# Kernel optimization log

Hardware: AMD Instinct MI355X
Metric: run time of the kernel (lower is better)

## Reference

```python
import jax, jax.numpy as jnp
import numpy as np

# ---- static config (matches init_kwargs) ----
B, NPG, C, L, H = 128, 256, 128, 3, 4   # graphs, nodes/graph, hidden, layers, heads
IN_CH, WALK, EDGE_IN, DEG = 30, 20, 11, 8
N = B * NPG
E = N * DEG
EPG = E // B                             # edges per graph
BN_EPS = 1e-5
HD = C // H


def setup_inputs() -> dict:
    key = jax.random.key(0)
    ks = list(jax.random.split(key, 80))
    ki = iter(ks)
    def w(shape, s=0.05):
        return jax.random.normal(next(ki), shape, jnp.float32) * s
    x = jax.random.normal(next(ki), (N, IN_CH), jnp.float32)
    # edges strictly within each graph (block-diagonal structure)
    src_l = jax.random.randint(next(ki), (E,), 0, NPG)
    dst_l = jax.random.randint(next(ki), (E,), 0, NPG)
    eg = jnp.repeat(jnp.arange(B, dtype=jnp.int32), EPG)
    edge_index = jnp.stack([eg * NPG + src_l.astype(jnp.int32),
                            eg * NPG + dst_l.astype(jnp.int32)])
    edge_attr = jax.random.normal(next(ki), (E, EDGE_IN), jnp.float32)
    batch = jnp.repeat(jnp.arange(B, dtype=jnp.int32), NPG)
    # all Linear weights stored [in, out] so y = x @ W + b
    inp = dict(x=x, edge_attr=edge_attr,
        in_W=w((IN_CH + WALK, C)), in_b=jnp.zeros((C,)),
        ep_W=w((EDGE_IN, C)), ep_b=jnp.zeros((C,)),
        ge_W=w((L, C, C)), ge_b=jnp.zeros((L, C)),          # GINE edge lin
        g1_W=w((L, C, C)), g1_b=jnp.zeros((L, C)),          # GINE nn layer1
        g2_W=w((L, C, C)), g2_b=jnp.zeros((L, C)),          # GINE nn layer2
        qkv_W=w((L, C, 3 * C)), qkv_b=jnp.zeros((L, 3 * C)),
        o_W=w((L, C, C)), o_b=jnp.zeros((L, C)),
        bn1_g=jnp.ones((L, C)), bn1_b=jnp.zeros((L, C)), bn1_m=w((L, C), 0.1), bn1_v=jnp.ones((L, C)),
        bn2_g=jnp.ones((L, C)), bn2_b=jnp.zeros((L, C)), bn2_m=w((L, C), 0.1), bn2_v=jnp.ones((L, C)),
        bn3_g=jnp.ones((L, C)), bn3_b=jnp.zeros((L, C)), bn3_m=w((L, C), 0.1), bn3_v=jnp.ones((L, C)),
        m1_W=w((L, C, 2 * C)), m1_b=jnp.zeros((L, 2 * C)),  # GPS ff block
        m2_W=w((L, 2 * C, C)), m2_b=jnp.zeros((L, C)),
        h1_W=w((C, 64)), h1_b=jnp.zeros((64,)),
        h2_W=w((64, 1)), h2_b=jnp.zeros((1,)),
        edge_index=edge_index, batch=batch)
    return inp


def _bn(x, g, b, m, v):  # BatchNorm1d, inference mode
    return (x - m) * jax.lax.rsqrt(v + BN_EPS) * g + b


def _rwse(edge_index):
    """diag of k-step random-walk matrix per graph; [N, WALK]."""
    src, dst = edge_index
    g = src // NPG
    A = jnp.zeros((B, NPG, NPG), jnp.float32).at[g, src % NPG, dst % NPG].add(1.0)
    A = A + jnp.eye(NPG, dtype=jnp.float32)          # add_self_loops
    deg = jnp.clip(jnp.sum(A, axis=-1), 1.0)         # out-degree of source
    M = jnp.swapaxes(A / deg[..., None], -1, -2)     # M[c,r] = A[r,c]/deg[r]
    p0 = jnp.broadcast_to(jnp.eye(NPG, dtype=jnp.float32), (B, NPG, NPG))
    def step(p, _):
        p = jnp.einsum('bcr,brn->bcn', M, p)
        return p, jnp.diagonal(p, axis1=-2, axis2=-1)
    _, diags = jax.lax.scan(step, p0, None, length=WALK)  # [WALK, B, NPG]
    return jnp.transpose(diags, (1, 2, 0)).reshape(N, WALK)


def _forward(x, edge_attr, in_W, in_b, ep_W, ep_b, ge_W, ge_b, g1_W, g1_b, g2_W, g2_b,
             qkv_W, qkv_b, o_W, o_b,
             bn1_g, bn1_b, bn1_m, bn1_v, bn2_g, bn2_b, bn2_m, bn2_v, bn3_g, bn3_b, bn3_m, bn3_v,
             m1_W, m1_b, m2_W, m2_b, h1_W, h1_b, h2_W, h2_b, edge_index, batch):
    pe = _rwse(edge_index)
    h = jnp.concatenate([x, pe], axis=-1) @ in_W + in_b      # input_proj
    e_emb = edge_attr @ ep_W + ep_b                          # edge_proj (dim==11)
    src, dst = edge_index[0], edge_index[1]
    for i in range(L):
        # --- GINEConv: relu(x_j + lin(edge)) -> scatter-sum -> MLP; eps=0 ---
        e = e_emb @ ge_W[i] + ge_b[i]
        msg = jax.nn.relu(h[src] + e)
        aggr = jax.ops.segment_sum(msg, dst, num_segments=N)
        loc = jax.nn.relu((h + aggr) @ g1_W[i] + g1_b[i]) @ g2_W[i] + g2_b[i]
        h1 = _bn(loc + h, bn1_g[i], bn1_b[i], bn1_m[i], bn1_v[i])
        # --- global multi-head attention on dense batch (uniform n, no padding) ---
        hd = h.reshape(B, NPG, C)
        qkv = hd @ qkv_W[i] + qkv_b[i]
        q, k, v = jnp.split(qkv, 3, axis=-1)
        q = q.reshape(B, NPG, H, HD); k = k.reshape(B, NPG, H, HD); v = v.reshape(B, NPG, H, HD)
        scores = jnp.einsum('bqhd,bkhd->bhqk', q, k) * (HD ** -0.5)
        attn = jax.nn.softmax(scores, axis=-1)
        o = jnp.einsum('bhqk,bkhd->bqhd', attn, v).reshape(B, NPG, C)
        o = (o @ o_W[i] + o_b[i]).reshape(N, C)
        h2 = _bn(o + h, bn2_g[i], bn2_b[i], bn2_m[i], bn2_v[i])
        # --- combine + feed-forward block ---
        out = h1 + h2
        ff = jax.nn.relu(out @ m1_W[i] + m1_b[i]) @ m2_W[i] + m2_b[i]
        h = _bn(out + ff, bn3_g[i], bn3_b[i], bn3_m[i], bn3_v[i])
    # --- global mean pool + head ---
    cnt = jax.ops.segment_sum(jnp.ones((N,), jnp.float32), batch, num_segments=B)
    pooled = jax.ops.segment_sum(h, batch, num_segments=B) / cnt[:, None]
    out = jax.nn.relu(pooled @ h1_W + h1_b) @ h2_W + h2_b
    return out[:, 0]  # [B]


def reference(x, edge_attr, in_W, in_b, ep_W, ep_b, ge_W, ge_b, g1_W, g1_b, g2_W, g2_b,
              qkv_W, qkv_b, o_W, o_b,
              bn1_g, bn1_b, bn1_m, bn1_v, bn2_g, bn2_b, bn2_m, bn2_v, bn3_g, bn3_b, bn3_m, bn3_v,
              m1_W, m1_b, m2_W, m2_b, h1_W, h1_b, h2_W, h2_b, edge_index, batch):
    return _forward(x, edge_attr, in_W, in_b, ep_W, ep_b, ge_W, ge_b, g1_W, g1_b, g2_W, g2_b,
                    qkv_W, qkv_b, o_W, o_b,
                    bn1_g, bn1_b, bn1_m, bn1_v, bn2_g, bn2_b, bn2_m, bn2_v, bn3_g, bn3_b, bn3_m, bn3_v,
                    m1_W, m1_b, m2_W, m2_b, h1_W, h1_b, h2_W, h2_b, edge_index, batch)
```

## Files before the change

### kernel.cpp

```cpp
#include <hip/hip_runtime.h>

#define GN   128
#define GP   256
#define NN   32768
#define NEDGE 262144
#define WALKN 20

typedef __attribute__((ext_vector_type(8))) short bfrag;
typedef __attribute__((ext_vector_type(4))) float ffrag;

__device__ __forceinline__ ushort f2b(float f){
  unsigned u = __float_as_uint(f);
  u += 0x7fffu + ((u >> 16) & 1u);
  return (ushort)(u >> 16);
}

__global__ __launch_bounds__(256) void build_edges(const int* __restrict__ ei, float* __restrict__ A,
                                                   int* __restrict__ epos, int* __restrict__ Ecnt){
  int e = blockIdx.x*256 + threadIdx.x;
  int s = ei[e], d = ei[NEDGE + e];
  int g = s >> 8;
  atomicAdd(&A[((size_t)g<<16) + ((size_t)(s&255)<<8) + (size_t)(d&255)], 1.0f);
  epos[e] = atomicAdd(&Ecnt[d], 1);
}

__global__ __launch_bounds__(256) void pack_edges(const int* __restrict__ ei, const float* __restrict__ ea,
                                                  const int* __restrict__ epos, float* __restrict__ pk){
  int e = blockIdx.x*256 + threadIdx.x;
  int d = ei[NEDGE + e];
  int pos = epos[e];
  if (pos >= 32) return;
  float* dst = pk + ((size_t)d*32 + pos)*12;
  dst[0] = __int_as_float(ei[e]);
  const float* s = ea + (size_t)e*11;
  #pragma unroll
  for (int t = 0; t < 11; t++) dst[1+t] = s[t];
}

__global__ __launch_bounds__(256) void rwse_deg(float* __restrict__ A, float* __restrict__ deg){
  int g = blockIdx.x, r = threadIdx.x;
  float* row = A + ((size_t)g<<16) + ((size_t)r<<8);
  row[r] += 1.0f;
  float s = 0.f;
  for (int c = 0; c < 256; c += 4){
    float4 v = *(const float4*)&row[c];
    s += v.x + v.y + v.z + v.w;
  }
  deg[(g<<8)+r] = fmaxf(s, 1.0f);
}

__global__ __launch_bounds__(256) void prep_m(const float* __restrict__ A, const float* __restrict__ deg,
                                              ushort* __restrict__ Mbf){
  __shared__ float As[64][65];
  __shared__ float Bs[64][65];
  __shared__ float invd[256];
  int g = blockIdx.x;
  const float* Ag = A + ((size_t)g<<16);
  int tid = threadIdx.x, tx = tid & 63, ty = tid >> 6;
  invd[tid] = 1.f / deg[(g<<8)+tid];
  ushort* Mg = Mbf + ((size_t)g<<16);
  const int pr[10] = {0,0,0,0,1,1,1,2,2,3};
  const int pc[10] = {0,1,2,3,1,2,3,2,3,3};
  for (int t = 0; t < 10; t++){
    int R0 = pr[t]*64, C0 = pc[t]*64;
    __syncthreads();
    #pragma unroll
    for (int i = 0; i < 16; i++){
      As[ty + i*4][tx] = Ag[(size_t)(R0 + ty + i*4)*256 + C0 + tx];
      Bs[ty + i*4][tx] = Ag[(size_t)(C0 + ty + i*4)*256 + R0 + tx];
    }
    __syncthreads();
    #pragma unroll
    for (int i = 0; i < 16; i++){
      int cl = ty + i*4;
      Mg[(size_t)(C0+cl)*256 + R0+tx] = f2b(As[tx][cl] * invd[R0+tx]);
      if (R0 != C0)
        Mg[(size_t)(R0+cl)*256 + C0+tx] = f2b(Bs[tx][cl] * invd[C0+tx]);
    }
  }
}

__global__ __launch_bounds__(256, 2) void rwse_mf(const ushort* __restrict__ Mbf,
                                                  float* __restrict__ pe){
  __shared__ __align__(16) ushort Pt[64*264];
  int bid = blockIdx.x;
  int g  = (bid & 7)*16 + (bid >> 5);
  int cb = ((bid >> 3) & 3) << 6;
  int tid = threadIdx.x, lane = tid & 63, w = tid >> 6;
  int l15 = lane & 15, quad = lane >> 4;
  const ushort* Mg = Mbf + ((size_t)g << 16);
  uint4 z4; z4.x = z4.y = z4.z = z4.w = 0u;
  for (int i = tid; i < 2112; i += 256) reinterpret_cast<uint4*>(Pt)[i] = z4;
  __syncthreads();
  if (tid < 64) Pt[tid*264 + cb + tid] = 0x3F80;
  __syncthreads();

  for (int s = 0; s < WALKN; s++){
    ffrag acc[4][4];
    #pragma unroll
    for (int mi = 0; mi < 4; mi++)
      #pragma unroll
      for (int n = 0; n < 4; n++) acc[mi][n] = (ffrag){0.f,0.f,0.f,0.f};
    for (int k0 = 0; k0 < 256; k0 += 32){
      bfrag a[4], b[4];
      #pragma unroll
      for (int mi = 0; mi < 4; mi++)
        a[mi] = *reinterpret_cast<const bfrag*>(&Mg[(size_t)(w*64 + mi*16 + l15)*256 + k0 + quad*8]);
      #pragma unroll
      for (int n = 0; n < 4; n++)
        b[n] = *reinterpret_cast<const bfrag*>(&Pt[(n*16 + l15)*264 + k0 + quad*8]);
      #pragma unroll
      for (int mi = 0; mi < 4; mi++)
        #pragma unroll
        for (int n = 0; n < 4; n++)
          acc[mi][n] = __builtin_amdgcn_mfma_f32_16x16x32_bf16(a[mi], b[n], acc[mi][n], 0, 0, 0);
    }
    __syncthreads();
    #pragma unroll
    for (int mi = 0; mi < 4; mi++){
      int rbase = w*64 + mi*16 + quad*4;
      #pragma unroll
      for (int n = 0; n < 4; n++){
        int cl = n*16 + l15;
        int dd = cb + cl - rbase;
        if (dd >= 0 && dd < 4){
          float dv = (dd==0)?acc[mi][n][0]:(dd==1)?acc[mi][n][1]:(dd==2)?acc[mi][n][2]:acc[mi][n][3];
          pe[(size_t)((g<<8) + cb + cl)*WALKN + s] = dv;
        }
        ushort4 pkk;
        pkk.x = f2b(acc[mi][n][0]); pkk.y = f2b(acc[mi][n][1]);
        pkk.z = f2b(acc[mi][n][2]); pkk.w = f2b(acc[mi][n][3]);
        *reinterpret_cast<ushort4*>(&Pt[cl*264 + rbase]) = pkk;
      }
    }
    __syncthreads();
  }
}

__global__ __launch_bounds__(256) void concat_kernel(const float* __restrict__ x, const float* __restrict__ pe,
                                                     float* __restrict__ xin){
  int idx = blockIdx.x*256 + threadIdx.x;
  int row = idx >> 6, c = idx & 63;
  float v = 0.f;
  if (c < 30) v = x[(size_t)row*30 + c];
  else if (c < 50) v = pe[(size_t)row*20 + (c-30)];
  xin[idx] = v;
}

__global__ __launch_bounds__(256) void prep_wt(const float* __restrict__ in_W, const float* __restrict__ g1_W,
                                               const float* __restrict__ g2_W, const float* __restrict__ qkv_W,
                                               const float* __restrict__ o_W, const float* __restrict__ m1_W,
                                               const float* __restrict__ m2_W, ushort* __restrict__ wt){
  int rgn = blockIdx.y;
  const float* src; int K, N, Kp; size_t dst;
  if (rgn == 0){ src = in_W; K=50; N=128; Kp=64; dst = 0; }
  else if (rgn <= 3){ int i=rgn-1;  src = g1_W + (size_t)i*16384; K=128; N=128; Kp=128; dst = 8192   + (size_t)i*16384; }
  else if (rgn <= 6){ int i=rgn-4;  src = g2_W + (size_t)i*16384; K=128; N=128; Kp=128; dst = 57344  + (size_t)i*16384; }
  else if (rgn <= 9){ int i=rgn-7;  src = qkv_W+ (size_t)i*49152; K=128; N=384; Kp=128; dst = 106496 + (size_t)i*49152; }
  else if (rgn <= 12){ int i=rgn-10; src = o_W  + (size_t)i*16384; K=128; N=128; Kp=128; dst = 253952 + (size_t)i*16384; }
  else if (rgn <= 15){ int i=rgn-13; src = m1_W + (size_t)i*32768; K=128; N=256; Kp=128; dst = 303104 + (size_t)i*32768; }
  else               { int i=rgn-16; src = m2_W + (size_t)i*32768; K=256; N=128; Kp=256; dst = 401408 + (size_t)i*32768; }
  int sz = N * Kp;
  int idx = blockIdx.x*256 + threadIdx.x;
  if (idx >= sz) return;
  int n = idx / Kp, kp = idx - n*Kp;
  float v = (kp < K) ? src[(size_t)kp*N + n] : 0.f;
  wt[dst + idx] = f2b(v);
}

template<int CINP, bool RELU, bool BN, bool HAS_X2, bool HAS_R, bool HAS_R2>
__global__ __launch_bounds__(256, 2) void gemm_mf(
    const float* __restrict__ X1, const float* __restrict__ X2,
    const ushort* __restrict__ WT, const float* __restrict__ bias,
    const float* __restrict__ Rp, const float* __restrict__ R2p,
    const float* __restrict__ bng, const float* __restrict__ bnb,
    const float* __restrict__ bnm, const float* __restrict__ bnv,
    float* __restrict__ Y, int ldY, int colTiles)
{
  constexpr int KT = (CINP > 128) ? 128 : CINP;
  constexpr int XS = KT + 8;
  __shared__ ushort XA[64 * XS];
  __shared__ ushort WS[128 * XS];
  int bt = blockIdx.x;
  int row0 = (bt / colTiles) * 64;
  int c0   = (bt % colTiles) * 128;
  int tid = threadIdx.x;
  int lane = tid & 63, wave = tid >> 6;
  int l15 = lane & 15, quad = lane >> 4;
  int wr = wave >> 1, wc = wave & 1;

  ffrag acc[2][4];
  #pragma unroll
  for (int m = 0; m < 2; m++)
    #pragma unroll
    for (int n = 0; n < 4; n++)
      acc[m][n] = (ffrag){0.f,0.f,0.f,0.f};

  #pragma unroll
  for (int s = 0; s < CINP/KT; s++){
    constexpr int F4PR = KT/4;
    #pragma unroll
    for (int it = 0; it < (64*F4PR)/256; it++){
      int idx = tid + it*256;
      int r = idx / F4PR, c4 = idx % F4PR;
      float4 v = *(const float4*)&X1[(size_t)(row0+r)*CINP + s*KT + c4*4];
      if (HAS_X2){
        float4 w = *(const float4*)&X2[(size_t)(row0+r)*CINP + s*KT + c4*4];
        v.x += w.x; v.y += w.y; v.z += w.z; v.w += w.w;
      }
      ushort4 b; b.x = f2b(v.x); b.y = f2b(v.y); b.z = f2b(v.z); b.w = f2b(v.w);
      *reinterpret_cast<ushort4*>(&XA[r*XS + c4*4]) = b;
    }
    constexpr int U4PR = KT/8;
    #pragma unroll
    for (int it = 0; it < (128*U4PR)/256; it++){
      int idx = tid + it*256;
      int n = idx / U4PR, c8 = idx % U4PR;
      uint4 v = *(const uint4*)&WT[(size_t)(c0+n)*CINP + s*KT + c8*8];
      *reinterpret_cast<uint4*>(&WS[n*XS + c8*8]) = v;
    }
    __syncthreads();
    #pragma unroll
    for (int ks = 0; ks < KT/32; ks++){
      bfrag a[2], b[4];
      #pragma unroll
      for (int m = 0; m < 2; m++)
        a[m] = *reinterpret_cast<const bfrag*>(&XA[(32*wr + 16*m + l15)*XS + ks*32 + quad*8]);
      #pragma unroll
      for (int n = 0; n < 4; n++)
        b[n] = *reinterpret_cast<const bfrag*>(&WS[(64*wc + 16*n + l15)*XS + ks*32 + quad*8]);
      #pragma unroll
      for (int m = 0; m < 2; m++)
        #pragma unroll
        for (int n = 0; n < 4; n++)
          acc[m][n] = __builtin_amdgcn_mfma_f32_16x16x32_bf16(a[m], b[n], acc[m][n], 0, 0, 0);
    }
    __syncthreads();
  }
  #pragma unroll
  for (int m = 0; m < 2; m++)
    #pragma unroll
    for (int n = 0; n < 4; n++){
      int col = c0 + 64*wc + 16*n + l15;
      float bs = bias[col];
      float bnscale = 0.f, bnsh = 0.f;
      if (BN){ bnscale = rsqrtf(bnv[col] + 1e-5f) * bng[col]; bnsh = bnb[col] - bnm[col]*bnscale; }
      #pragma unroll
      for (int rg = 0; rg < 4; rg++){
        int r = row0 + 32*wr + 16*m + quad*4 + rg;
        float v = acc[m][n][rg] + bs;
        if (RELU) v = fmaxf(v, 0.f);
        if (HAS_R) v += Rp[(size_t)r*ldY + col];
        if (BN)   v = v*bnscale + bnsh;
        if (HAS_R2) v += R2p[(size_t)r*ldY + col];
        Y[(size_t)r*ldY + col] = v;
      }
    }
}

__global__ __launch_bounds__(256) void wp_all(const float* __restrict__ epW, const float* __restrict__ epb,
                                              const float* __restrict__ geW, const float* __restrict__ geb,
                                              float* __restrict__ Wp, float* __restrict__ bp){
  int i = blockIdx.x;
  const float* gw = geW + (size_t)i*16384;
  float* wp = Wp + (size_t)i*1408;
  int tid = threadIdx.x;
  for (int idx = tid; idx < 1408; idx += 256){
    int t = idx >> 7, c = idx & 127;
    float s = 0.f;
    for (int k = 0; k < 128; k++) s += epW[t*128+k] * gw[(size_t)k*128 + c];
    wp[idx] = s;
  }
  if (tid < 128){
    float s = geb[(size_t)i*128 + tid];
    for (int k = 0; k < 128; k++) s += epb[k] * gw[(size_t)k*128 + tid];
    bp[(size_t)i*128 + tid] = s;
  }
}

__global__ __launch_bounds__(256) void gine_aggr2(const float* __restrict__ h, const float* __restrict__ pk,
                                                  const int* __restrict__ Ecnt,
                                                  const float* __restrict__ Wp, const float* __restrict__ bp,
                                                  float* __restrict__ aggr){
  int n = blockIdx.x*2 + (threadIdx.x >> 7);
  int ch = threadIdx.x & 127;
  int cnt = Ecnt[n]; if (cnt > 32) cnt = 32;
  float wreg[11];
  #pragma unroll
  for (int t = 0; t < 11; t++) wreg[t] = Wp[t*128 + ch];
  float bpc = bp[ch];
  const float* pkn = pk + (size_t)n*384;
  float acc = 0.f;
  int j = 0;
  for (; j + 4 <= cnt; j += 4){
    const float* p0 = pkn + (size_t)(j+0)*12;
    const float* p1 = pkn + (size_t)(j+1)*12;
    const float* p2 = pkn + (size_t)(j+2)*12;
    const float* p3 = pkn + (size_t)(j+3)*12;
    int s0 = __float_as_int(p0[0]), s1 = __float_as_int(p1[0]);
    int s2 = __float_as_int(p2[0]), s3 = __float_as_int(p3[0]);
    float h0 = h[(size_t)s0*128 + ch];
    float h1 = h[(size_t)s1*128 + ch];
    float h2 = h[(size_t)s2*128 + ch];
    float h3 = h[(size_t)s3*128 + ch];
    float e0 = bpc, e1 = bpc, e2 = bpc, e3 = bpc;
    #pragma unroll
    for (int t = 0; t < 11; t++){
      e0 += p0[1+t]*wreg[t]; e1 += p1[1+t]*wreg[t];
      e2 += p2[1+t]*wreg[t]; e3 += p3[1+t]*wreg[t];
    }
    acc += fmaxf(h0+e0, 0.f) + fmaxf(h1+e1, 0.f) + fmaxf(h2+e2, 0.f) + fmaxf(h3+e3, 0.f);
  }
  for (; j < cnt; j++){
    const float* p0 = pkn + (size_t)j*12;
    int s0 = __float_as_int(p0[0]);
    float h0 = h[(size_t)s0*128 + ch];
    float e0 = bpc;
    #pragma unroll
    for (int t = 0; t < 11; t++) e0 += p0[1+t]*wreg[t];
    acc += fmaxf(h0+e0, 0.f);
  }
  aggr[(size_t)n*128 + ch] = acc;
}

__global__ __launch_bounds__(256, 2) void attn_mf(const float* __restrict__ qkv, float* __restrict__ o){
  __shared__ ushort Ks[256 * 40];
  __shared__ ushort Vt[32 * 264];
  __shared__ ushort PA[4 * 16 * 264];
  int g = blockIdx.x >> 2, hh = blockIdx.x & 3;
  int tid = threadIdx.x, lane = tid & 63, w = tid >> 6;
  int l15 = lane & 15, quad = lane >> 4;
  const float* base = qkv + (size_t)(g<<8)*384;

  #pragma unroll
  for (int it = 0; it < 8; it++){
    int idx = tid + it*256;
    int key = idx >> 3, d4 = idx & 7;
    float4 kv = *(const float4*)&base[(size_t)key*384 + 128 + hh*32 + d4*4];
    ushort4 kb; kb.x=f2b(kv.x); kb.y=f2b(kv.y); kb.z=f2b(kv.z); kb.w=f2b(kv.w);
    *reinterpret_cast<ushort4*>(&Ks[key*40 + d4*4]) = kb;
    float4 vv = *(const float4*)&base[(size_t)key*384 + 256 + hh*32 + d4*4];
    Vt[(d4*4+0)*264 + key] = f2b(vv.x);
    Vt[(d4*4+1)*264 + key] = f2b(vv.y);
    Vt[(d4*4+2)*264 + key] = f2b(vv.z);
    Vt[(d4*4+3)*264 + key] = f2b(vv.w);
  }
  bfrag qf[4];
  #pragma unroll
  for (int qg = 0; qg < 4; qg++){
    int q = w*64 + qg*16 + l15;
    const float* qp = base + (size_t)q*384 + hh*32 + quad*8;
    float4 v0 = *(const float4*)qp;
    float4 v1 = *(const float4*)(qp + 4);
    bfrag t;
    t[0]=(short)f2b(v0.x); t[1]=(short)f2b(v0.y); t[2]=(short)f2b(v0.z); t[3]=(short)f2b(v0.w);
    t[4]=(short)f2b(v1.x); t[5]=(short)f2b(v1.y); t[6]=(short)f2b(v1.z); t[7]=(short)f2b(v1.w);
    qf[qg] = t;
  }
  __syncthreads();

  ushort* pw = &PA[w * 16 * 264];
  const float sc_ = 0.17677669529663687f;
  for (int qg = 0; qg < 4; qg++){
    ffrag sc[16];
    #pragma unroll
    for (int kg = 0; kg < 16; kg++){
      bfrag bk = *reinterpret_cast<const bfrag*>(&Ks[(kg*16 + l15)*40 + quad*8]);
      ffrag z = (ffrag){0.f,0.f,0.f,0.f};
      sc[kg] = __builtin_amdgcn_mfma_f32_16x16x32_bf16(qf[qg], bk, z, 0, 0, 0);
    }
    float inv_l[4];
    #pragma unroll
    for (int rg = 0; rg < 4; rg++){
      float m = sc[0][rg];
      #pragma unroll
      for (int kg = 1; kg < 16; kg++) m = fmaxf(m, sc[kg][rg]);
      #pragma unroll
      for (int off = 1; off < 16; off <<= 1) m = fmaxf(m, __shfl_xor(m, off, 16));
      float ssum = 0.f;
      #pragma unroll
      for (int kg = 0; kg < 16; kg++){
        float p = __expf((sc[kg][rg] - m) * sc_);
        sc[kg][rg] = p; ssum += p;
      }
      #pragma unroll
      for (int off = 1; off < 16; off <<= 1) ssum += __shfl_xor(ssum, off, 16);
      inv_l[rg] = 1.f / ssum;
    }
    #pragma unroll
    for (int kg = 0; kg < 16; kg++)
      #pragma unroll
      for (int rg = 0; rg < 4; rg++)
        pw[(quad*4 + rg)*264 + kg*16 + l15] = f2b(sc[kg][rg]);
    ffrag oa[2];
    oa[0] = (ffrag){0.f,0.f,0.f,0.f};
    oa[1] = (ffrag){0.f,0.f,0.f,0.f};
    #pragma unroll
    for (int ks = 0; ks < 8; ks++){
      bfrag pa = *reinterpret_cast<const bfrag*>(&pw[l15*264 + ks*32 + quad*8]);
      #pragma unroll
      for (int n16 = 0; n16 < 2; n16++){
        bfrag bv = *reinterpret_cast<const bfrag*>(&Vt[(n16*16 + l15)*264 + ks*32 + quad*8]);
        oa[n16] = __builtin_amdgcn_mfma_f32_16x16x32_bf16(pa, bv, oa[n16], 0, 0, 0);
      }
    }
    #pragma unroll
    for (int n16 = 0; n16 < 2; n16++)
      #pragma unroll
      for (int rg = 0; rg < 4; rg++){
        int q = w*64 + qg*16 + quad*4 + rg;
        int col = hh*32 + n16*16 + l15;
        o[((size_t)(g<<8) + q)*128 + col] = oa[n16][rg] * inv_l[rg];
      }
  }
}

__global__ __launch_bounds__(256) void head_kernel(const float* __restrict__ h,
                                                   const float* __restrict__ W1, const float* __restrict__ b1,
                                                   const float* __restrict__ W2, const float* __restrict__ b2,
                                                   float* __restrict__ out){
  int g = blockIdx.x, tid = threadIdx.x;
  int c = tid & 127, half = tid >> 7;
  __shared__ float part[2][128];
  __shared__ float pool[128];
  __shared__ float hid[64];
  float s = 0.f;
  for (int n = half*128; n < half*128 + 128; n++)
    s += h[(size_t)((g<<8)+n)*128 + c];
  part[half][c] = s;
  __syncthreads();
  if (tid < 128) pool[tid] = (part[0][tid] + part[1][tid]) * (1.f/256.f);
  __syncthreads();
  if (tid < 64){
    float v = b1[tid];
    for (int k = 0; k < 128; k++) v += pool[k] * W1[k*64 + tid];
    hid[tid] = fmaxf(v, 0.f);
  }
  __syncthreads();
  if (tid == 0){
    float v = b2[0];
    for (int k = 0; k < 64; k++) v += hid[k] * W2[k];
    out[g] = v;
  }
}

extern "C" void kernel_launch(void* const* d_in, const int* in_sizes, int n_in,
                              void* d_out, int out_size, void* d_ws, size_t ws_size,
                              hipStream_t stream){
  (void)in_sizes; (void)n_in; (void)out_size; (void)ws_size;
  const float* x      = (const float*)d_in[0];
  const float* eattr  = (const float*)d_in[1];
  const float* in_W   = (const float*)d_in[2];
  const float* in_b   = (const float*)d_in[3];
  const float* ep_W   = (const float*)d_in[4];
  const float* ep_b   = (const float*)d_in[5];
  const float* ge_W   = (const float*)d_in[6];
  const float* ge_b   = (const float*)d_in[7];
  const float* g1_W   = (const float*)d_in[8];
  const float* g1_b   = (const float*)d_in[9];
  const float* g2_W   = (const float*)d_in[10];
  const float* g2_b   = (const float*)d_in[11];
  const float* qkv_W  = (const float*)d_in[12];
  const float* qkv_b  = (const float*)d_in[13];
  const float* o_W    = (const float*)d_in[14];
  const float* o_b    = (const float*)d_in[15];
  const float* bn1g = (const float*)d_in[16]; const float* bn1b = (const float*)d_in[17];
  const float* bn1m = (const float*)d_in[18]; const float* bn1v = (const float*)d_in[19];
  const float* bn2g = (const float*)d_in[20]; const float* bn2b = (const float*)d_in[21];
  const float* bn2m = (const float*)d_in[22]; const float* bn2v = (const float*)d_in[23];
  const float* bn3g = (const float*)d_in[24]; const float* bn3b = (const float*)d_in[25];
  const float* bn3m = (const float*)d_in[26]; const float* bn3v = (const float*)d_in[27];
  const float* m1_W = (const float*)d_in[28]; const float* m1_b = (const float*)d_in[29];
  const float* m2_W = (const float*)d_in[30]; const float* m2_b = (const float*)d_in[31];
  const float* h1_W = (const float*)d_in[32]; const float* h1_b = (const float*)d_in[33];
  const float* h2_W = (const float*)d_in[34]; const float* h2_b = (const float*)d_in[35];
  const int*   ei   = (const int*)d_in[36];
  float* out = (float*)d_out;
  float* ws  = (float*)d_ws;
  int*   wsi = (int*)d_ws;

  const size_t oA    = 0;
  const size_t oMbf  = 8388608;
  const size_t oXin  = 0;
  const size_t oQKV  = 0;
  const size_t oT2   = 0;
  const size_t oPk   = 12582912;
  const size_t oDeg  = 25165824;
  const size_t oPe   = 25198592;
  const size_t oH    = 25853952;
  const size_t oB1   = 30048256;
  const size_t oHO   = 34242560;
  const size_t oWp   = 38436864;
  const size_t oBp   = 38441088;
  const size_t oEpos = 38441472;
  const size_t oEcnt = 38703616;
  const size_t oWT   = 38736384;
  ushort* wt  = (ushort*)(ws + oWT);
  ushort* mbf = (ushort*)(ws + oMbf);

  hipMemsetAsync(ws + oA, 0, 8388608*sizeof(float), stream);
  hipMemsetAsync(wsi + oEcnt, 0, 32768*sizeof(int), stream);
  build_edges<<<NEDGE/256, 256, 0, stream>>>(ei, ws+oA, wsi+oEpos, wsi+oEcnt);
  pack_edges<<<NEDGE/256, 256, 0, stream>>>(ei, eattr, wsi+oEpos, ws+oPk);
  rwse_deg<<<GN, 256, 0, stream>>>(ws+oA, ws+oDeg);
  prep_m<<<GN, 256, 0, stream>>>(ws+oA, ws+oDeg, mbf);
  rwse_mf<<<GN*4, 256, 0, stream>>>(mbf, ws+oPe);

  prep_wt<<<dim3(192, 19), 256, 0, stream>>>(in_W, g1_W, g2_W, qkv_W, o_W, m1_W, m2_W, wt);

  concat_kernel<<<NN*64/256, 256, 0, stream>>>(x, ws+oPe, ws+oXin);
  gemm_mf<64,false,false,false,false,false><<<512, 256, 0, stream>>>(
      ws+oXin, nullptr, wt + 0, in_b, nullptr, nullptr, nullptr, nullptr, nullptr, nullptr,
      ws+oH, 128, 1);

  wp_all<<<3, 256, 0, stream>>>(ep_W, ep_b, ge_W, ge_b, ws+oWp, ws+oBp);

  for (int i = 0; i < 3; i++){
    gine_aggr2<<<NN/2, 256, 0, stream>>>(ws+oH, ws+oPk, wsi+oEcnt,
                                         ws+oWp + (size_t)i*1408, ws+oBp + (size_t)i*128, ws+oB1);
    gemm_mf<128,true,false,true,false,false><<<512, 256, 0, stream>>>(
        ws+oH, ws+oB1, wt + 8192 + (size_t)i*16384, g1_b + (size_t)i*128,
        nullptr, nullptr, nullptr, nullptr, nullptr, nullptr, ws+oB1, 128, 1);
    gemm_mf<128,false,true,false,true,false><<<512, 256, 0, stream>>>(
        ws+oB1, nullptr, wt + 57344 + (size_t)i*16384, g2_b + (size_t)i*128,
        ws+oH, nullptr, bn1g+(size_t)i*128, bn1b+(size_t)i*128, bn1m+(size_t)i*128, bn1v+(size_t)i*128,
        ws+oHO, 128, 1);
    gemm_mf<128,false,false,false,false,false><<<1536, 256, 0, stream>>>(
        ws+oH, nullptr, wt + 106496 + (size_t)i*49152, qkv_b + (size_t)i*384,
        nullptr, nullptr, nullptr, nullptr, nullptr, nullptr, ws+oQKV, 384, 3);
    attn_mf<<<GN*4, 256, 0, stream>>>(ws+oQKV, ws+oB1);
    gemm_mf<128,false,true,false,true,true><<<512, 256, 0, stream>>>(
        ws+oB1, nullptr, wt + 253952 + (size_t)i*16384, o_b + (size_t)i*128,
        ws+oH, ws+oHO, bn2g+(size_t)i*128, bn2b+(size_t)i*128, bn2m+(size_t)i*128, bn2v+(size_t)i*128,
        ws+oHO, 128, 1);
    gemm_mf<128,true,false,false,false,false><<<1024, 256, 0, stream>>>(
        ws+oHO, nullptr, wt + 303104 + (size_t)i*32768, m1_b + (size_t)i*256,
        nullptr, nullptr, nullptr, nullptr, nullptr, nullptr, ws+oT2, 256, 2);
    gemm_mf<256,false,true,false,true,false><<<512, 256, 0, stream>>>(
        ws+oT2, nullptr, wt + 401408 + (size_t)i*32768, m2_b + (size_t)i*128,
        ws+oHO, nullptr, bn3g+(size_t)i*128, bn3b+(size_t)i*128, bn3m+(size_t)i*128, bn3v+(size_t)i*128,
        ws+oH, 128, 1);
  }

  head_kernel<<<GN, 256, 0, stream>>>(ws+oH, h1_W, h1_b, h2_W, h2_b, out);
}
```

Measured before the change: 825.3 us.

## Store activations in bf16 and fuse GINE MLP and attention-output/FF GEMM chains

Switches intermediate activations (hidden state, QKV, attention output, aggregation) from fp32 to bf16 storage, halving memory traffic in gathers and GEMM loads. Fuses the two GINE MLP GEMMs into one kernel and the out-projection, FF1 and FF2 GEMMs into another, keeping intermediates in shared memory. This removes several launches and global round-trips at the cost of large LDS use (occupancy 1 for the FF kernel) and extra bf16 rounding error.

Result: faster. 737.7 us (-10.6%).

```diff
diff --git a/kernel.cpp b/kernel.cpp
--- a/kernel.cpp
+++ b/kernel.cpp
@@ -13,6 +13,14 @@
   unsigned u = __float_as_uint(f);
   u += 0x7fffu + ((u >> 16) & 1u);
   return (ushort)(u >> 16);
+}
+__device__ __forceinline__ float b2f(ushort u){
+  return __uint_as_float(((unsigned)u) << 16);
+}
+__device__ __forceinline__ unsigned addpair(unsigned a, unsigned b){
+  float alo = __uint_as_float(a << 16), ahi = __uint_as_float(a & 0xffff0000u);
+  float blo = __uint_as_float(b << 16), bhi = __uint_as_float(b & 0xffff0000u);
+  return ((unsigned)f2b(ahi + bhi) << 16) | (unsigned)f2b(alo + blo);
 }
 
 __global__ __launch_bounds__(256) void build_edges(const int* __restrict__ ei, float* __restrict__ A,
@@ -138,13 +146,13 @@
 }
 
 __global__ __launch_bounds__(256) void concat_kernel(const float* __restrict__ x, const float* __restrict__ pe,
-                                                     float* __restrict__ xin){
+                                                     ushort* __restrict__ xinb){
   int idx = blockIdx.x*256 + threadIdx.x;
   int row = idx >> 6, c = idx & 63;
   float v = 0.f;
   if (c < 30) v = x[(size_t)row*30 + c];
   else if (c < 50) v = pe[(size_t)row*20 + (c-30)];
-  xin[idx] = v;
+  xinb[idx] = f2b(v);
 }
 
 __global__ __launch_bounds__(256) void prep_wt(const float* __restrict__ in_W, const float* __restrict__ g1_W,
@@ -168,17 +176,12 @@
   wt[dst + idx] = f2b(v);
 }
 
-template<int CINP, bool RELU, bool BN, bool HAS_X2, bool HAS_R, bool HAS_R2>
-__global__ __launch_bounds__(256, 2) void gemm_mf(
-    const float* __restrict__ X1, const float* __restrict__ X2,
-    const ushort* __restrict__ WT, const float* __restrict__ bias,
-    const float* __restrict__ Rp, const float* __restrict__ R2p,
-    const float* __restrict__ bng, const float* __restrict__ bnb,
-    const float* __restrict__ bnm, const float* __restrict__ bnv,
-    float* __restrict__ Y, int ldY, int colTiles)
+template<int CINP>
+__global__ __launch_bounds__(256, 2) void gemm_b(
+    const ushort* __restrict__ X1, const ushort* __restrict__ WT,
+    const float* __restrict__ bias, ushort* __restrict__ Y, int ldY, int colTiles)
 {
-  constexpr int KT = (CINP > 128) ? 128 : CINP;
-  constexpr int XS = KT + 8;
+  constexpr int XS = CINP + 8;
   __shared__ ushort XA[64 * XS];
   __shared__ ushort WS[128 * XS];
   int bt = blockIdx.x;
@@ -188,54 +191,42 @@
   int lane = tid & 63, wave = tid >> 6;
   int l15 = lane & 15, quad = lane >> 4;
   int wr = wave >> 1, wc = wave & 1;
-
+  constexpr int C8 = CINP/8;
+
+  #pragma unroll
+  for (int it = 0; it < CINP/32; it++){
+    int idx = tid + it*256;
+    int r = idx / C8, c8 = (idx % C8)*8;
+    *reinterpret_cast<uint4*>(&XA[r*XS + c8]) =
+        *reinterpret_cast<const uint4*>(&X1[(size_t)(row0+r)*CINP + c8]);
+  }
+  #pragma unroll
+  for (int it = 0; it < CINP/16; it++){
+    int idx = tid + it*256;
+    int n = idx / C8, c8 = (idx % C8)*8;
+    *reinterpret_cast<uint4*>(&WS[n*XS + c8]) =
+        *reinterpret_cast<const uint4*>(&WT[(size_t)(c0+n)*CINP + c8]);
+  }
+  __syncthreads();
   ffrag acc[2][4];
   #pragma unroll
   for (int m = 0; m < 2; m++)
     #pragma unroll
+    for (int n = 0; n < 4; n++) acc[m][n] = (ffrag){0.f,0.f,0.f,0.f};
+  #pragma unroll
+  for (int ks = 0; ks < CINP/32; ks++){
+    bfrag a[2], b[4];
+    #pragma unroll
+    for (int m = 0; m < 2; m++)
+      a[m] = *reinterpret_cast<const bfrag*>(&XA[(32*wr + 16*m + l15)*XS + ks*32 + quad*8]);
+    #pragma unroll
     for (int n = 0; n < 4; n++)
-      acc[m][n] = (ffrag){0.f,0.f,0.f,0.f};
-
-  #pragma unroll
-  for (int s = 0; s < CINP/KT; s++){
-    constexpr int F4PR = KT/4;
-    #pragma unroll
-    for (int it = 0; it < (64*F4PR)/256; it++){
-      int idx = tid + it*256;
-      int r = idx / F4PR, c4 = idx % F4PR;
-      float4 v = *(const float4*)&X1[(size_t)(row0+r)*CINP + s*KT + c4*4];
-      if (HAS_X2){
-        float4 w = *(const float4*)&X2[(size_t)(row0+r)*CINP + s*KT + c4*4];
-        v.x += w.x; v.y += w.y; v.z += w.z; v.w += w.w;
-      }
-      ushort4 b; b.x = f2b(v.x); b.y = f2b(v.y); b.z = f2b(v.z); b.w = f2b(v.w);
-      *reinterpret_cast<ushort4*>(&XA[r*XS + c4*4]) = b;
-    }
-    constexpr int U4PR = KT/8;
-    #pragma unroll
-    for (int it = 0; it < (128*U4PR)/256; it++){
-      int idx = tid + it*256;
-      int n = idx / U4PR, c8 = idx % U4PR;
-      uint4 v = *(const uint4*)&WT[(size_t)(c0+n)*CINP + s*KT + c8*8];
-      *reinterpret_cast<uint4*>(&WS[n*XS + c8*8]) = v;
-    }
-    __syncthreads();
-    #pragma unroll
-    for (int ks = 0; ks < KT/32; ks++){
-      bfrag a[2], b[4];
-      #pragma unroll
-      for (int m = 0; m < 2; m++)
-        a[m] = *reinterpret_cast<const bfrag*>(&XA[(32*wr + 16*m + l15)*XS + ks*32 + quad*8]);
+      b[n] = *reinterpret_cast<const bfrag*>(&WS[(64*wc + 16*n + l15)*XS + ks*32 + quad*8]);
+    #pragma unroll
+    for (int m = 0; m < 2; m++)
       #pragma unroll
       for (int n = 0; n < 4; n++)
-        b[n] = *reinterpret_cast<const bfrag*>(&WS[(64*wc + 16*n + l15)*XS + ks*32 + quad*8]);
-      #pragma unroll
-      for (int m = 0; m < 2; m++)
-        #pragma unroll
-        for (int n = 0; n < 4; n++)
-          acc[m][n] = __builtin_amdgcn_mfma_f32_16x16x32_bf16(a[m], b[n], acc[m][n], 0, 0, 0);
-    }
-    __syncthreads();
+        acc[m][n] = __builtin_amdgcn_mfma_f32_16x16x32_bf16(a[m], b[n], acc[m][n], 0, 0, 0);
   }
   #pragma unroll
   for (int m = 0; m < 2; m++)
@@ -243,17 +234,278 @@
     for (int n = 0; n < 4; n++){
       int col = c0 + 64*wc + 16*n + l15;
       float bs = bias[col];
-      float bnscale = 0.f, bnsh = 0.f;
-      if (BN){ bnscale = rsqrtf(bnv[col] + 1e-5f) * bng[col]; bnsh = bnb[col] - bnm[col]*bnscale; }
       #pragma unroll
       for (int rg = 0; rg < 4; rg++){
         int r = row0 + 32*wr + 16*m + quad*4 + rg;
-        float v = acc[m][n][rg] + bs;
-        if (RELU) v = fmaxf(v, 0.f);
-        if (HAS_R) v += Rp[(size_t)r*ldY + col];
-        if (BN)   v = v*bnscale + bnsh;
-        if (HAS_R2) v += R2p[(size_t)r*ldY + col];
-        Y[(size_t)r*ldY + col] = v;
+        Y[(size_t)r*ldY + col] = f2b(acc[m][n][rg] + bs);
+      }
+    }
+}
+
+__global__ __launch_bounds__(256, 2) void gine_mlp(
+    const ushort* __restrict__ hb, const ushort* __restrict__ agb,
+    const ushort* __restrict__ w1, const float* __restrict__ b1v,
+    const ushort* __restrict__ w2, const float* __restrict__ b2v,
+    const float* __restrict__ bng, const float* __restrict__ bnb,
+    const float* __restrict__ bnm, const float* __restrict__ bnv,
+    ushort* __restrict__ h1b)
+{
+  __shared__ ushort XA[64*136];
+  __shared__ ushort WS[128*136];
+  __shared__ ushort T1[64*136];
+  int row0 = blockIdx.x * 64;
+  int tid = threadIdx.x, lane = tid & 63, wave = tid >> 6;
+  int l15 = lane & 15, quad = lane >> 4;
+  int wr = wave >> 1, wc = wave & 1;
+
+  #pragma unroll
+  for (int it = 0; it < 4; it++){
+    int idx = tid + it*256;
+    int r = idx >> 4, c8 = (idx & 15)*8;
+    uint4 av = *reinterpret_cast<const uint4*>(&hb[(size_t)(row0+r)*128 + c8]);
+    uint4 bv = *reinterpret_cast<const uint4*>(&agb[(size_t)(row0+r)*128 + c8]);
+    uint4 o; o.x=addpair(av.x,bv.x); o.y=addpair(av.y,bv.y); o.z=addpair(av.z,bv.z); o.w=addpair(av.w,bv.w);
+    *reinterpret_cast<uint4*>(&XA[r*136 + c8]) = o;
+  }
+  #pragma unroll
+  for (int it = 0; it < 8; it++){
+    int idx = tid + it*256;
+    int n = idx >> 4, c8 = (idx & 15)*8;
+    *reinterpret_cast<uint4*>(&WS[n*136 + c8]) =
+        *reinterpret_cast<const uint4*>(&w1[(size_t)n*128 + c8]);
+  }
+  __syncthreads();
+  ffrag acc[2][4];
+  #pragma unroll
+  for (int m = 0; m < 2; m++)
+    #pragma unroll
+    for (int n = 0; n < 4; n++) acc[m][n] = (ffrag){0.f,0.f,0.f,0.f};
+  #pragma unroll
+  for (int ks = 0; ks < 4; ks++){
+    bfrag a[2], b[4];
+    #pragma unroll
+    for (int m = 0; m < 2; m++)
+      a[m] = *reinterpret_cast<const bfrag*>(&XA[(32*wr + 16*m + l15)*136 + ks*32 + quad*8]);
+    #pragma unroll
+    for (int n = 0; n < 4; n++)
+      b[n] = *reinterpret_cast<const bfrag*>(&WS[(64*wc + 16*n + l15)*136 + ks*32 + quad*8]);
+    #pragma unroll
+    for (int m = 0; m < 2; m++)
+      #pragma unroll
+      for (int n = 0; n < 4; n++)
+        acc[m][n] = __builtin_amdgcn_mfma_f32_16x16x32_bf16(a[m], b[n], acc[m][n], 0, 0, 0);
+  }
+  __syncthreads();
+  #pragma unroll
+  for (int m = 0; m < 2; m++)
+    #pragma unroll
+    for (int n = 0; n < 4; n++){
+      int col = 64*wc + 16*n + l15;
+      float bs = b1v[col];
+      #pragma unroll
+      for (int rg = 0; rg < 4; rg++){
+        int rl = 32*wr + 16*m + quad*4 + rg;
+        T1[rl*136 + col] = f2b(fmaxf(acc[m][n][rg] + bs, 0.f));
+      }
+    }
+  #pragma unroll
+  for (int it = 0; it < 8; it++){
+    int idx = tid + it*256;
+    int n = idx >> 4, c8 = (idx & 15)*8;
+    *reinterpret_cast<uint4*>(&WS[n*136 + c8]) =
+        *reinterpret_cast<const uint4*>(&w2[(size_t)n*128 + c8]);
+  }
+  __syncthreads();
+  #pragma unroll
+  for (int m = 0; m < 2; m++)
+    #pragma unroll
+    for (int n = 0; n < 4; n++) acc[m][n] = (ffrag){0.f,0.f,0.f,0.f};
+  #pragma unroll
+  for (int ks = 0; ks < 4; ks++){
+    bfrag a[2], b[4];
+    #pragma unroll
+    for (int m = 0; m < 2; m++)
+      a[m] = *reinterpret_cast<const bfrag*>(&T1[(32*wr + 16*m + l15)*136 + ks*32 + quad*8]);
+    #pragma unroll
+    for (int n = 0; n < 4; n++)
+      b[n] = *reinterpret_cast<const bfrag*>(&WS[(64*wc + 16*n + l15)*136 + ks*32 + quad*8]);
+    #pragma unroll
+    for (int m = 0; m < 2; m++)
+      #pragma unroll
+      for (int n = 0; n < 4; n++)
+        acc[m][n] = __builtin_amdgcn_mfma_f32_16x16x32_bf16(a[m], b[n], acc[m][n], 0, 0, 0);
+  }
+  #pragma unroll
+  for (int m = 0; m < 2; m++)
+    #pragma unroll
+    for (int n = 0; n < 4; n++){
+      int col = 64*wc + 16*n + l15;
+      float bs = b2v[col];
+      float sc = rsqrtf(bnv[col] + 1e-5f) * bng[col];
+      float sh = bnb[col] - bnm[col]*sc;
+      #pragma unroll
+      for (int rg = 0; rg < 4; rg++){
+        int r = row0 + 32*wr + 16*m + quad*4 + rg;
+        float v = acc[m][n][rg] + bs + b2f(hb[(size_t)r*128 + col]);
+        h1b[(size_t)r*128 + col] = f2b(v*sc + sh);
+      }
+    }
+}
+
+__global__ __launch_bounds__(256, 1) void ff_fused(
+    const ushort* __restrict__ obb, const ushort* __restrict__ hb, const ushort* __restrict__ h1b,
+    const ushort* __restrict__ wo, const float* __restrict__ ob_b,
+    const float* __restrict__ bn2g, const float* __restrict__ bn2b,
+    const float* __restrict__ bn2m, const float* __restrict__ bn2v,
+    const ushort* __restrict__ wm1, const float* __restrict__ m1b,
+    const ushort* __restrict__ wm2, const float* __restrict__ m2b,
+    const float* __restrict__ bn3g, const float* __restrict__ bn3b,
+    const float* __restrict__ bn3m, const float* __restrict__ bn3v,
+    ushort* __restrict__ hout)
+{
+  __shared__ ushort XA[64*136];
+  __shared__ ushort WS[256*136];
+  __shared__ ushort OUT[64*136];
+  __shared__ ushort T2[64*264];
+  int row0 = blockIdx.x * 64;
+  int tid = threadIdx.x, lane = tid & 63, wave = tid >> 6;
+  int l15 = lane & 15, quad = lane >> 4;
+  int wr = wave >> 1, wc = wave & 1;
+
+  #pragma unroll
+  for (int it = 0; it < 4; it++){
+    int idx = tid + it*256;
+    int r = idx >> 4, c8 = (idx & 15)*8;
+    *reinterpret_cast<uint4*>(&XA[r*136 + c8]) =
+        *reinterpret_cast<const uint4*>(&obb[(size_t)(row0+r)*128 + c8]);
+  }
+  #pragma unroll
+  for (int it = 0; it < 8; it++){
+    int idx = tid + it*256;
+    int n = idx >> 4, c8 = (idx & 15)*8;
+    *reinterpret_cast<uint4*>(&WS[n*136 + c8]) =
+        *reinterpret_cast<const uint4*>(&wo[(size_t)n*128 + c8]);
+  }
+  __syncthreads();
+  ffrag acc[2][4];
+  #pragma unroll
+  for (int m = 0; m < 2; m++)
+    #pragma unroll
+    for (int n = 0; n < 4; n++) acc[m][n] = (ffrag){0.f,0.f,0.f,0.f};
+  #pragma unroll
+  for (int ks = 0; ks < 4; ks++){
+    bfrag a[2], b[4];
+    #pragma unroll
+    for (int m = 0; m < 2; m++)
+      a[m] = *reinterpret_cast<const bfrag*>(&XA[(32*wr + 16*m + l15)*136 + ks*32 + quad*8]);
+    #pragma unroll
+    for (int n = 0; n < 4; n++)
+      b[n] = *reinterpret_cast<const bfrag*>(&WS[(64*wc + 16*n + l15)*136 + ks*32 + quad*8]);
+    #pragma unroll
+    for (int m = 0; m < 2; m++)
+      #pragma unroll
+      for (int n = 0; n < 4; n++)
+        acc[m][n] = __builtin_amdgcn_mfma_f32_16x16x32_bf16(a[m], b[n], acc[m][n], 0, 0, 0);
+  }
+  __syncthreads();
+  #pragma unroll
+  for (int m = 0; m < 2; m++)
+    #pragma unroll
+    for (int n = 0; n < 4; n++){
+      int col = 64*wc + 16*n + l15;
+      float bs = ob_b[col];
+      float sc = rsqrtf(bn2v[col] + 1e-5f) * bn2g[col];
+      float sh = bn2b[col] - bn2m[col]*sc;
+      #pragma unroll
+      for (int rg = 0; rg < 4; rg++){
+        int rl = 32*wr + 16*m + quad*4 + rg;
+        int r = row0 + rl;
+        float v = acc[m][n][rg] + bs + b2f(hb[(size_t)r*128 + col]);
+        v = v*sc + sh + b2f(h1b[(size_t)r*128 + col]);
+        OUT[rl*136 + col] = f2b(v);
+      }
+    }
+  #pragma unroll
+  for (int it = 0; it < 16; it++){
+    int idx = tid + it*256;
+    int n = idx >> 4, c8 = (idx & 15)*8;
+    *reinterpret_cast<uint4*>(&WS[n*136 + c8]) =
+        *reinterpret_cast<const uint4*>(&wm1[(size_t)n*128 + c8]);
+  }
+  __syncthreads();
+  ffrag acc2[2][8];
+  #pragma unroll
+  for (int m = 0; m < 2; m++)
+    #pragma unroll
+    for (int n = 0; n < 8; n++) acc2[m][n] = (ffrag){0.f,0.f,0.f,0.f};
+  #pragma unroll
+  for (int ks = 0; ks < 4; ks++){
+    bfrag a[2], b[8];
+    #pragma unroll
+    for (int m = 0; m < 2; m++)
+      a[m] = *reinterpret_cast<const bfrag*>(&OUT[(32*wr + 16*m + l15)*136 + ks*32 + quad*8]);
+    #pragma unroll
+    for (int n = 0; n < 8; n++)
+      b[n] = *reinterpret_cast<const bfrag*>(&WS[(128*wc + 16*n + l15)*136 + ks*32 + quad*8]);
+    #pragma unroll
+    for (int m = 0; m < 2; m++)
+      #pragma unroll
+      for (int n = 0; n < 8; n++)
+        acc2[m][n] = __builtin_amdgcn_mfma_f32_16x16x32_bf16(a[m], b[n], acc2[m][n], 0, 0, 0);
+  }
+  __syncthreads();
+  #pragma unroll
+  for (int m = 0; m < 2; m++)
+    #pragma unroll
+    for (int n = 0; n < 8; n++){
+      int col = 128*wc + 16*n + l15;
+      float bs = m1b[col];
+      #pragma unroll
+      for (int rg = 0; rg < 4; rg++){
+        int rl = 32*wr + 16*m + quad*4 + rg;
+        T2[rl*264 + col] = f2b(fmaxf(acc2[m][n][rg] + bs, 0.f));
+      }
+    }
+  #pragma unroll
+  for (int it = 0; it < 16; it++){
+    int idx = tid + it*256;
+    int n = idx >> 5, c8 = (idx & 31)*8;
+    *reinterpret_cast<uint4*>(&WS[n*264 + c8]) =
+        *reinterpret_cast<const uint4*>(&wm2[(size_t)n*256 + c8]);
+  }
+  __syncthreads();
+  #pragma unroll
+  for (int m = 0; m < 2; m++)
+    #pragma unroll
+    for (int n = 0; n < 4; n++) acc[m][n] = (ffrag){0.f,0.f,0.f,0.f};
+  #pragma unroll
+  for (int ks = 0; ks < 8; ks++){
+    bfrag a[2], b[4];
+    #pragma unroll
+    for (int m = 0; m < 2; m++)
+      a[m] = *reinterpret_cast<const bfrag*>(&T2[(32*wr + 16*m + l15)*264 + ks*32 + quad*8]);
+    #pragma unroll
+    for (int n = 0; n < 4; n++)
+      b[n] = *reinterpret_cast<const bfrag*>(&WS[(64*wc + 16*n + l15)*264 + ks*32 + quad*8]);
+    #pragma unroll
+    for (int m = 0; m < 2; m++)
+      #pragma unroll
+      for (int n = 0; n < 4; n++)
+        acc[m][n] = __builtin_amdgcn_mfma_f32_16x16x32_bf16(a[m], b[n], acc[m][n], 0, 0, 0);
+  }
+  #pragma unroll
+  for (int m = 0; m < 2; m++)
+    #pragma unroll
+    for (int n = 0; n < 4; n++){
+      int col = 64*wc + 16*n + l15;
+      float bs = m2b[col];
+      float sc = rsqrtf(bn3v[col] + 1e-5f) * bn3g[col];
+      float sh = bn3b[col] - bn3m[col]*sc;
+      #pragma unroll
+      for (int rg = 0; rg < 4; rg++){
+        int rl = 32*wr + 16*m + quad*4 + rg;
+        float v = acc[m][n][rg] + bs + b2f(OUT[rl*136 + col]);
+        hout[(size_t)(row0+rl)*128 + col] = f2b(v*sc + sh);
       }
     }
 }
@@ -278,10 +530,10 @@
   }
 }
 
-__global__ __launch_bounds__(256) void gine_aggr2(const float* __restrict__ h, const float* __restrict__ pk,
+__global__ __launch_bounds__(256) void gine_aggr2(const ushort* __restrict__ hb, const float* __restrict__ pk,
                                                   const int* __restrict__ Ecnt,
                                                   const float* __restrict__ Wp, const float* __restrict__ bp,
-                                                  float* __restrict__ aggr){
+                                                  ushort* __restrict__ agb){
   int n = blockIdx.x*2 + (threadIdx.x >> 7);
   int ch = threadIdx.x & 127;
   int cnt = Ecnt[n]; if (cnt > 32) cnt = 32;
@@ -299,10 +551,10 @@
     const float* p3 = pkn + (size_t)(j+3)*12;
     int s0 = __float_as_int(p0[0]), s1 = __float_as_int(p1[0]);
     int s2 = __float_as_int(p2[0]), s3 = __float_as_int(p3[0]);
-    float h0 = h[(size_t)s0*128 + ch];
-    float h1 = h[(size_t)s1*128 + ch];
-    float h2 = h[(size_t)s2*128 + ch];
-    float h3 = h[(size_t)s3*128 + ch];
+    float h0 = b2f(hb[(size_t)s0*128 + ch]);
+    float h1 = b2f(hb[(size_t)s1*128 + ch]);
+    float h2 = b2f(hb[(size_t)s2*128 + ch]);
+    float h3 = b2f(hb[(size_t)s3*128 + ch]);
     float e0 = bpc, e1 = bpc, e2 = bpc, e3 = bpc;
     #pragma unroll
     for (int t = 0; t < 11; t++){
@@ -314,48 +566,40 @@
   for (; j < cnt; j++){
     const float* p0 = pkn + (size_t)j*12;
     int s0 = __float_as_int(p0[0]);
-    float h0 = h[(size_t)s0*128 + ch];
+    float h0 = b2f(hb[(size_t)s0*128 + ch]);
     float e0 = bpc;
     #pragma unroll
     for (int t = 0; t < 11; t++) e0 += p0[1+t]*wreg[t];
     acc += fmaxf(h0+e0, 0.f);
   }
-  aggr[(size_t)n*128 + ch] = acc;
-}
-
-__global__ __launch_bounds__(256, 2) void attn_mf(const float* __restrict__ qkv, float* __restrict__ o){
+  agb[(size_t)n*128 + ch] = f2b(acc);
+}
+
+__global__ __launch_bounds__(256, 2) void attn_mf(const ushort* __restrict__ qkvb, ushort* __restrict__ obb){
   __shared__ ushort Ks[256 * 40];
   __shared__ ushort Vt[32 * 264];
   __shared__ ushort PA[4 * 16 * 264];
   int g = blockIdx.x >> 2, hh = blockIdx.x & 3;
   int tid = threadIdx.x, lane = tid & 63, w = tid >> 6;
   int l15 = lane & 15, quad = lane >> 4;
-  const float* base = qkv + (size_t)(g<<8)*384;
-
-  #pragma unroll
-  for (int it = 0; it < 8; it++){
-    int idx = tid + it*256;
-    int key = idx >> 3, d4 = idx & 7;
-    float4 kv = *(const float4*)&base[(size_t)key*384 + 128 + hh*32 + d4*4];
-    ushort4 kb; kb.x=f2b(kv.x); kb.y=f2b(kv.y); kb.z=f2b(kv.z); kb.w=f2b(kv.w);
-    *reinterpret_cast<ushort4*>(&Ks[key*40 + d4*4]) = kb;
-    float4 vv = *(const float4*)&base[(size_t)key*384 + 256 + hh*32 + d4*4];
-    Vt[(d4*4+0)*264 + key] = f2b(vv.x);
-    Vt[(d4*4+1)*264 + key] = f2b(vv.y);
-    Vt[(d4*4+2)*264 + key] = f2b(vv.z);
-    Vt[(d4*4+3)*264 + key] = f2b(vv.w);
+  const ushort* base = qkvb + (size_t)(g<<8)*384;
+
+  #pragma unroll
+  for (int it = 0; it < 4; it++){
+    int idx = tid + it*256;
+    int key = idx >> 2, d8 = (idx & 3)*8;
+    uint4 kv = *reinterpret_cast<const uint4*>(&base[(size_t)key*384 + 128 + hh*32 + d8]);
+    *reinterpret_cast<uint4*>(&Ks[key*40 + d8]) = kv;
+    uint4 vv = *reinterpret_cast<const uint4*>(&base[(size_t)key*384 + 256 + hh*32 + d8]);
+    const ushort* vp = reinterpret_cast<const ushort*>(&vv);
+    #pragma unroll
+    for (int t = 0; t < 8; t++) Vt[(d8+t)*264 + key] = vp[t];
   }
   bfrag qf[4];
   #pragma unroll
   for (int qg = 0; qg < 4; qg++){
     int q = w*64 + qg*16 + l15;
-    const float* qp = base + (size_t)q*384 + hh*32 + quad*8;
-    float4 v0 = *(const float4*)qp;
-    float4 v1 = *(const float4*)(qp + 4);
-    bfrag t;
-    t[0]=(short)f2b(v0.x); t[1]=(short)f2b(v0.y); t[2]=(short)f2b(v0.z); t[3]=(short)f2b(v0.w);
-    t[4]=(short)f2b(v1.x); t[5]=(short)f2b(v1.y); t[6]=(short)f2b(v1.z); t[7]=(short)f2b(v1.w);
-    qf[qg] = t;
+    qf[qg] = *reinterpret_cast<const bfrag*>(&base[(size_t)q*384 + hh*32 + quad*8]);
   }
   __syncthreads();
 
@@ -410,12 +654,12 @@
       for (int rg = 0; rg < 4; rg++){
         int q = w*64 + qg*16 + quad*4 + rg;
         int col = hh*32 + n16*16 + l15;
-        o[((size_t)(g<<8) + q)*128 + col] = oa[n16][rg] * inv_l[rg];
-      }
-  }
-}
-
-__global__ __launch_bounds__(256) void head_kernel(const float* __restrict__ h,
+        obb[((size_t)(g<<8) + q)*128 + col] = f2b(oa[n16][rg] * inv_l[rg]);
+      }
+  }
+}
+
+__global__ __launch_bounds__(256) void head_kernel(const ushort* __restrict__ hb,
                                                    const float* __restrict__ W1, const float* __restrict__ b1,
                                                    const float* __restrict__ W2, const float* __restrict__ b2,
                                                    float* __restrict__ out){
@@ -426,7 +670,7 @@
   __shared__ float hid[64];
   float s = 0.f;
   for (int n = half*128; n < half*128 + 128; n++)
-    s += h[(size_t)((g<<8)+n)*128 + c];
+    s += b2f(hb[(size_t)((g<<8)+n)*128 + c]);
   part[half][c] = s;
   __syncthreads();
   if (tid < 128) pool[tid] = (part[0][tid] + part[1][tid]) * (1.f/256.f);
@@ -481,22 +725,24 @@
 
   const size_t oA    = 0;
   const size_t oMbf  = 8388608;
-  const size_t oXin  = 0;
-  const size_t oQKV  = 0;
-  const size_t oT2   = 0;
   const size_t oPk   = 12582912;
   const size_t oDeg  = 25165824;
   const size_t oPe   = 25198592;
-  const size_t oH    = 25853952;
-  const size_t oB1   = 30048256;
-  const size_t oHO   = 34242560;
-  const size_t oWp   = 38436864;
-  const size_t oBp   = 38441088;
-  const size_t oEpos = 38441472;
-  const size_t oEcnt = 38703616;
-  const size_t oWT   = 38736384;
-  ushort* wt  = (ushort*)(ws + oWT);
-  ushort* mbf = (ushort*)(ws + oMbf);
+  const size_t oHb   = 25853952;
+  const size_t oH1b  = 27951104;
+  const size_t oBb   = 30048256;
+  const size_t oWp   = 32145408;
+  const size_t oBp   = 32149632;
+  const size_t oEpos = 32150016;
+  const size_t oEcnt = 32412160;
+  const size_t oWT   = 32444928;
+  ushort* wt   = (ushort*)(ws + oWT);
+  ushort* mbf  = (ushort*)(ws + oMbf);
+  ushort* xinb = (ushort*)(ws + 0);
+  ushort* qkvb = (ushort*)(ws + 0);
+  ushort* hb   = (ushort*)(ws + oHb);
+  ushort* h1b  = (ushort*)(ws + oH1b);
+  ushort* bbuf = (ushort*)(ws + oBb);
 
   hipMemsetAsync(ws + oA, 0, 8388608*sizeof(float), stream);
   hipMemsetAsync(wsi + oEcnt, 0, 32768*sizeof(int), stream);
@@ -508,39 +754,30 @@
 
   prep_wt<<<dim3(192, 19), 256, 0, stream>>>(in_W, g1_W, g2_W, qkv_W, o_W, m1_W, m2_W, wt);
 
-  concat_kernel<<<NN*64/256, 256, 0, stream>>>(x, ws+oPe, ws+oXin);
-  gemm_mf<64,false,false,false,false,false><<<512, 256, 0, stream>>>(
-      ws+oXin, nullptr, wt + 0, in_b, nullptr, nullptr, nullptr, nullptr, nullptr, nullptr,
-      ws+oH, 128, 1);
+  concat_kernel<<<NN*64/256, 256, 0, stream>>>(x, ws+oPe, xinb);
+  gemm_b<64><<<512, 256, 0, stream>>>(xinb, wt + 0, in_b, hb, 128, 1);
 
   wp_all<<<3, 256, 0, stream>>>(ep_W, ep_b, ge_W, ge_b, ws+oWp, ws+oBp);
 
   for (int i = 0; i < 3; i++){
-    gine_aggr2<<<NN/2, 256, 0, stream>>>(ws+oH, ws+oPk, wsi+oEcnt,
-                                         ws+oWp + (size_t)i*1408, ws+oBp + (size_t)i*128, ws+oB1);
-    gemm_mf<128,true,false,true,false,false><<<512, 256, 0, stream>>>(
-        ws+oH, ws+oB1, wt + 8192 + (size_t)i*16384, g1_b + (size_t)i*128,
-        nullptr, nullptr, nullptr, nullptr, nullptr, nullptr, ws+oB1, 128, 1);
-    gemm_mf<128,false,true,false,true,false><<<512, 256, 0, stream>>>(
-        ws+oB1, nullptr, wt + 57344 + (size_t)i*16384, g2_b + (size_t)i*128,
-        ws+oH, nullptr, bn1g+(size_t)i*128, bn1b+(size_t)i*128, bn1m+(size_t)i*128, bn1v+(size_t)i*128,
-        ws+oHO, 128, 1);
-    gemm_mf<128,false,false,false,false,false><<<1536, 256, 0, stream>>>(
-        ws+oH, nullptr, wt + 106496 + (size_t)i*49152, qkv_b + (size_t)i*384,
-        nullptr, nullptr, nullptr, nullptr, nullptr, nullptr, ws+oQKV, 384, 3);
-    attn_mf<<<GN*4, 256, 0, stream>>>(ws+oQKV, ws+oB1);
-    gemm_mf<128,false,true,false,true,true><<<512, 256, 0, stream>>>(
-        ws+oB1, nullptr, wt + 253952 + (size_t)i*16384, o_b + (size_t)i*128,
-        ws+oH, ws+oHO, bn2g+(size_t)i*128, bn2b+(size_t)i*128, bn2m+(size_t)i*128, bn2v+(size_t)i*128,
-        ws+oHO, 128, 1);
-    gemm_mf<128,true,false,false,false,false><<<1024, 256, 0, stream>>>(
-        ws+oHO, nullptr, wt + 303104 + (size_t)i*32768, m1_b + (size_t)i*256,
-        nullptr, nullptr, nullptr, nullptr, nullptr, nullptr, ws+oT2, 256, 2);
-    gemm_mf<256,false,true,false,true,false><<<512, 256, 0, stream>>>(
-        ws+oT2, nullptr, wt + 401408 + (size_t)i*32768, m2_b + (size_t)i*128,
-        ws+oHO, nullptr, bn3g+(size_t)i*128, bn3b+(size_t)i*128, bn3m+(size_t)i*128, bn3v+(size_t)i*128,
-        ws+oH, 128, 1);
-  }
-
-  head_kernel<<<GN, 256, 0, stream>>>(ws+oH, h1_W, h1_b, h2_W, h2_b, out);
-}
+    gine_aggr2<<<NN/2, 256, 0, stream>>>(hb, ws+oPk, wsi+oEcnt,
+                                         ws+oWp + (size_t)i*1408, ws+oBp + (size_t)i*128, bbuf);
+    gine_mlp<<<512, 256, 0, stream>>>(hb, bbuf,
+        wt + 8192 + (size_t)i*16384, g1_b + (size_t)i*128,
+        wt + 57344 + (size_t)i*16384, g2_b + (size_t)i*128,
+        bn1g+(size_t)i*128, bn1b+(size_t)i*128, bn1m+(size_t)i*128, bn1v+(size_t)i*128,
+        h1b);
+    gemm_b<128><<<1536, 256, 0, stream>>>(hb, wt + 106496 + (size_t)i*49152,
+                                          qkv_b + (size_t)i*384, qkvb, 384, 3);
+    attn_mf<<<GN*4, 256, 0, stream>>>(qkvb, bbuf);
+    ff_fused<<<512, 256, 0, stream>>>(bbuf, hb, h1b,
+        wt + 253952 + (size_t)i*16384, o_b + (size_t)i*128,
+        bn2g+(size_t)i*128, bn2b+(size_t)i*128, bn2m+(size_t)i*128, bn2v+(size_t)i*128,
+        wt + 303104 + (size_t)i*32768, m1_b + (size_t)i*256,
+        wt + 401408 + (size_t)i*32768, m2_b + (size_t)i*128,
+        bn3g+(size_t)i*128, bn3b+(size_t)i*128, bn3m+(size_t)i*128, bn3v+(size_t)i*128,
+        hb);
+  }
+
+  head_kernel<<<GN, 256, 0, stream>>>(hb, h1_W, h1_b, h2_W, h2_b, out);
+}
```
